# Kernel tuning notes

Measured on AMD Instinct MI355X. Metric: run time of the kernel, lower is better.

Reference implementation:

```python
import jax, jax.numpy as jnp
import numpy as np

SAMPLE_SIZE = 4096  # deterministic mode: first SAMPLE_SIZE flattened pixels
EPS_STD = 1e-8
EPS_PDF = 1e-10


def _std(v):
    # torch.std is unbiased (ddof=1)
    return jnp.std(v, ddof=1)


def _adaptive_sigma(v):
    # sigma=None path: 0.2 * std, clamped to [0.001, 1.0]
    return jnp.clip(_std(v) * 0.2, 0.001, 1.0)


def _normalize(v):
    return (v - jnp.mean(v)) / (_std(v) + EPS_STD)


def _marginal_pdf(values, sigma):
    vn = _normalize(values)                      # [N]
    resid = vn[None, :] - vn[:, None]            # [N, N]
    kernel = jnp.exp(-0.5 * (resid / sigma) ** 2)
    pdf = jnp.mean(kernel, axis=1)               # [N]
    return pdf / (jnp.sum(pdf) + EPS_PDF)


def _joint_pdf(v1, v2, s1, s2):
    vn1 = _normalize(v1)
    vn2 = _normalize(v2)
    r1 = vn1[None, :] - vn1[:, None]             # [N, N]
    r2 = vn2[None, :] - vn2[:, None]             # [N, N]
    kernel = jnp.exp(-0.5 * (r1 / s1) ** 2) * jnp.exp(-0.5 * (r2 / s2) ** 2)
    pdf = jnp.mean(kernel, axis=1)
    return pdf / (jnp.sum(pdf) + EPS_PDF)


def _mi_kde(img1, img2):
    x = img1.reshape(-1)[:SAMPLE_SIZE]
    y = img2.reshape(-1)[:SAMPLE_SIZE]
    s1 = _adaptive_sigma(x)
    s2 = _adaptive_sigma(y)
    p1 = _marginal_pdf(x, s1)
    p2 = _marginal_pdf(y, s2)
    pj = _joint_pdf(x, y, s1, s2)
    ratio = (pj + EPS_PDF) / (p1 * p2 + EPS_PDF)
    log_ratio = jnp.log(jnp.clip(ratio, 1e-10, 1e10))
    return jnp.sum(pj * log_ratio)


def setup_inputs() -> dict:
    key = jax.random.key(0)
    k1, k2, k3 = jax.random.split(key, 3)
    shape = (2, 1, 128, 128)  # [B, C, H, W] images in [0, 1]
    return {
        "fused_img": jax.random.uniform(k1, shape, dtype=jnp.float32),
        "source_img1": jax.random.uniform(k2, shape, dtype=jnp.float32),
        "source_img2": jax.random.uniform(k3, shape, dtype=jnp.float32),
    }


def reference(fused_img, source_img1, source_img2):
    B = fused_img.shape[0]
    total = jnp.float32(0.0)
    for b in range(B):  # small fixed batch loop, matches original
        total = total + _mi_kde(fused_img[b], source_img1[b]) \
                      + _mi_kde(fused_img[b], source_img2[b])
    return -(total / B)
```

## Files before the change

### kernel.cpp

```cpp
#include <hip/hip_runtime.h>

#define N 4096
#define NBIN 1024
#define LOG2E 1.4426950408889634f

__device__ __forceinline__ float fast_exp2(float x) {
#if __has_builtin(__builtin_amdgcn_exp2f)
    return __builtin_amdgcn_exp2f(x);
#else
    return exp2f(x);
#endif
}

__device__ float block_reduce_sum(float v) {
    __shared__ float red[16];
    int lane = threadIdx.x & 63;
    int wid = threadIdx.x >> 6;
    #pragma unroll
    for (int off = 32; off; off >>= 1) v += __shfl_down(v, off, 64);
    if (lane == 0) red[wid] = v;
    __syncthreads();
    if (threadIdx.x == 0) {
        int nw = (int)(blockDim.x >> 6);
        float s = red[0];
        for (int w = 1; w < nw; ++w) s += red[w];
        red[0] = s;
    }
    __syncthreads();
    float r = red[0];
    __syncthreads();
    return r;
}

__device__ float block_reduce_min(float v) {
    __shared__ float redm[16];
    int lane = threadIdx.x & 63;
    int wid = threadIdx.x >> 6;
    #pragma unroll
    for (int off = 32; off; off >>= 1) v = fminf(v, __shfl_down(v, off, 64));
    if (lane == 0) redm[wid] = v;
    __syncthreads();
    if (threadIdx.x == 0) {
        int nw = (int)(blockDim.x >> 6);
        float s = redm[0];
        for (int w = 1; w < nw; ++w) s = fminf(s, redm[w]);
        redm[0] = s;
    }
    __syncthreads();
    float r = redm[0];
    __syncthreads();
    return r;
}

__device__ float block_reduce_max(float v) {
    __shared__ float redx[16];
    int lane = threadIdx.x & 63;
    int wid = threadIdx.x >> 6;
    #pragma unroll
    for (int off = 32; off; off >>= 1) v = fmaxf(v, __shfl_down(v, off, 64));
    if (lane == 0) redx[wid] = v;
    __syncthreads();
    if (threadIdx.x == 0) {
        int nw = (int)(blockDim.x >> 6);
        float s = redx[0];
        for (int w = 1; w < nw; ++w) s = fmaxf(s, redx[w]);
        redx[0] = s;
    }
    __syncthreads();
    float r = redx[0];
    __syncthreads();
    return r;
}

__global__ void k_prep(const float* __restrict__ fused,
                       const float* __restrict__ s1,
                       const float* __restrict__ s2,
                       float2* __restrict__ xa,
                       float2* __restrict__ ma,
                       float* __restrict__ par,
                       float* __restrict__ hcnt,
                       float* __restrict__ hmu) {
    __shared__ unsigned int cnt[NBIN];
    __shared__ int qs[NBIN];
    int vec = blockIdx.x;
    int b = vec / 3, k = vec % 3;
    const float* src = (k == 0 ? fused : (k == 1 ? s1 : s2)) + b * 16384;
    int tid = threadIdx.x;
    float v[16];
    float s = 0.f;
    #pragma unroll
    for (int t = 0; t < 16; ++t) { v[t] = src[tid + t * 256]; s += v[t]; }
    float total = block_reduce_sum(s);
    float mean = total * (1.0f / 4096.0f);
    float ssq = 0.f;
    #pragma unroll
    for (int t = 0; t < 16; ++t) { float d = v[t] - mean; ssq += d * d; }
    float tssq = block_reduce_sum(ssq);
    float stdv = sqrtf(tssq / 4095.0f);
    float sigma = fminf(fmaxf(0.2f * stdv, 0.001f), 1.0f);
    float inv = 1.0f / (stdv + 1e-8f);
    float c1 = -0.5f * LOG2E / (sigma * sigma);

    float x[16];
    float lmin = 1e30f, lmax = -1e30f;
    #pragma unroll
    for (int t = 0; t < 16; ++t) {
        x[t] = (v[t] - mean) * inv;
        lmin = fminf(lmin, x[t]);
        lmax = fmaxf(lmax, x[t]);
    }
    float xmin = block_reduce_min(lmin);
    float xmax = block_reduce_max(lmax);
    float range = fmaxf(xmax - xmin, 1e-6f);
    float inv_bw = (float)NBIN / range;
    float binw = range * (1.0f / NBIN);

    float2* xav = xa + (size_t)vec * N;
    float2* mav = ma + (size_t)vec * N;
    for (int u = tid; u < NBIN; u += 256) { cnt[u] = 0u; qs[u] = 0; }
    __syncthreads();
    #pragma unroll
    for (int t = 0; t < 16; ++t) {
        int i = tid + t * 256;
        float a = c1 * x[t] * x[t];
        xav[i] = make_float2(x[t], a);
        mav[i] = make_float2(-2.0f * c1 * x[t], a);
        float rel = x[t] - xmin;
        int bb = min(NBIN - 1, max(0, (int)(rel * inv_bw)));
        atomicAdd(&cnt[bb], 1u);
        atomicAdd(&qs[bb], (int)rintf(rel * 16384.0f));
    }
    __syncthreads();
    for (int u = tid; u < NBIN; u += 256) {
        unsigned int c = cnt[u];
        hcnt[vec * NBIN + u] = (float)c;
        float mu = c ? xmin + ((float)qs[u] / (float)c) * (1.0f / 16384.0f)
                     : xmin + (u + 0.5f) * binw;
        hmu[vec * NBIN + u] = mu;
    }
    if (tid == 0) {
        par[vec * 8 + 0] = xmin;
        par[vec * 8 + 1] = inv_bw;
        par[vec * 8 + 2] = binw;
        par[vec * 8 + 3] = c1;
    }
}

__global__ void __launch_bounds__(256, 8)
k_main(const float2* __restrict__ xa,
       const float2* __restrict__ ma,
       const float* __restrict__ par,
       const float* __restrict__ hcnt,
       const float* __restrict__ hmu,
       float* __restrict__ marg,
       float* __restrict__ msum_part,
       float* __restrict__ part, int js) {
    __shared__ float4 sj[128];
    const int nib = 4;
    int bid = blockIdx.x;
    int tid = threadIdx.x;

    if (bid < 96) {
        int vec = bid >> 4, ic = bid & 15;
        int i = ic * 256 + tid;
        const float* P = par + vec * 8;
        float xmin = P[0], inv_bw = P[1], c1 = P[3];
        float xi = xa[(size_t)vec * N + i].x;
        float R = sqrtf(45.0f / fabsf(c1));
        int b0 = max(0, (int)((xi - R - xmin) * inv_bw));
        int b1 = min(NBIN - 1, (int)((xi + R - xmin) * inv_bw) + 1);
        const float* hc = hcnt + vec * NBIN;
        const float* hm = hmu + vec * NBIN;
        float acc = 0.f;
        #pragma unroll 4
        for (int bb = b0; bb <= b1; ++bb) {
            float d = xi - hm[bb];
            acc += hc[bb] * fast_exp2(c1 * d * d);
        }
        float raw = acc * (1.0f / N);
        marg[(size_t)vec * N + i] = raw;
        float tot = block_reduce_sum(raw);
        if (tid == 0) msum_part[bid] = tot;
        return;
    }

    int bid2 = bid - 96;
    int tt = bid2 / (nib * js);
    int rem = bid2 % (nib * js);
    int ib = rem / js, jsp = rem % js;
    int b = tt >> 1, pr = tt & 1;
    int vx = b * 3, vy = b * 3 + 1 + pr;
    int jlen = N / js;
    int j0 = jsp * jlen;
    int ibase = ib * 1024 + tid;

    const float2* xav = xa + (size_t)vx * N;
    const float2* yav = xa + (size_t)vy * N;
    const float2* mxv = ma + (size_t)vx * N;
    const float2* myv = ma + (size_t)vy * N;

    float mx[4], my[4], C[4];
    #pragma unroll
    for (int u = 0; u < 4; ++u) {
        float2 qx = mxv[ibase + u * 256];
        float2 qy = myv[ibase + u * 256];
        mx[u] = qx.x; my[u] = qy.x; C[u] = qx.y + qy.y;
    }
    float acc[4] = {0.f, 0.f, 0.f, 0.f};

    for (int jt = 0; jt < jlen; jt += 128) {
        int cnt = min(128, jlen - jt);
        __syncthreads();
        if (tid < cnt) {
            float2 xq = xav[j0 + jt + tid];
            float2 yq = yav[j0 + jt + tid];
            sj[tid] = make_float4(xq.x, yq.x, xq.y + yq.y, 0.f);
        }
        __syncthreads();
        #pragma unroll 2
        for (int j = 0; j < cnt; j += 2) {
            float4 q0 = sj[j];
            float4 q1 = sj[j + 1];
            float e0[4], e1[4], f0[4], f1[4];
            #pragma unroll
            for (int u = 0; u < 4; ++u) {
                e0[u] = fmaf(my[u], q0.y, fmaf(mx[u], q0.x, C[u])) + q0.z;
                e1[u] = fmaf(my[u], q1.y, fmaf(mx[u], q1.x, C[u])) + q1.z;
            }
            #pragma unroll
            for (int u = 0; u < 4; ++u) {
                f0[u] = fast_exp2(e0[u]);
                f1[u] = fast_exp2(e1[u]);
            }
            #pragma unroll
            for (int u = 0; u < 4; ++u)
                acc[u] += (f0[u] + f1[u]);
        }
    }
    float* dst = part + ((size_t)tt * js + jsp) * N + ibase;
    dst[0]   = acc[0];
    dst[256] = acc[1];
    dst[512] = acc[2];
    dst[768] = acc[3];
}

__global__ void k_reduce(const float* __restrict__ part, float* __restrict__ pdfj,
                         float* __restrict__ jsum_part, int js) {
    int blk = blockIdx.x;
    int tt = blk >> 4;
    int ic = blk & 15;
    int i = ic * 256 + threadIdx.x;
    float s = 0.f;
    #pragma unroll 4
    for (int q = 0; q < js; ++q) s += part[((size_t)tt * js + q) * N + i];
    s *= (1.0f / N);
    pdfj[(size_t)tt * N + i] = s;
    float tot = block_reduce_sum(s);
    if (threadIdx.x == 0) jsum_part[blk] = tot;
}

__global__ void k_mifin(const float* __restrict__ pdfj,
                        const float* __restrict__ jsum_part,
                        const float* __restrict__ marg,
                        const float* __restrict__ msum_part,
                        float* __restrict__ out) {
    __shared__ float tmp[160];
    __shared__ float svec[6], stask[4];
    int tid = threadIdx.x;
    if (tid < 96) tmp[tid] = msum_part[tid];
    else if (tid >= 128 && tid < 192) tmp[96 + tid - 128] = jsum_part[tid - 128];
    __syncthreads();
    if (tid < 6) {
        float s = 0.f;
        #pragma unroll
        for (int q = 0; q < 16; ++q) s += tmp[tid * 16 + q];
        svec[tid] = s;
    } else if (tid >= 8 && tid < 12) {
        int c = tid - 8;
        float s = 0.f;
        #pragma unroll
        for (int q = 0; q < 16; ++q) s += tmp[96 + c * 16 + q];
        stask[c] = s;
    }
    __syncthreads();

    float local = 0.f;
    #pragma unroll
    for (int k = 0; k < 16; ++k) {
        int g = tid + k * 1024;
        int c = g >> 12;
        int i = g & 4095;
        int b = c >> 1, pr = c & 1;
        int vx = b * 3, vy = b * 3 + 1 + pr;
        float pj = pdfj[(size_t)c * N + i] / (stask[c] + 1e-10f);
        float px = marg[(size_t)vx * N + i] / (svec[vx] + 1e-10f);
        float py = marg[(size_t)vy * N + i] / (svec[vy] + 1e-10f);
        float ratio = (pj + 1e-10f) / (px * py + 1e-10f);
        ratio = fminf(fmaxf(ratio, 1e-10f), 1e10f);
        local += pj * __logf(ratio);
    }
    float tot = block_reduce_sum(local);
    if (tid == 0) out[0] = -tot * 0.5f;
}

extern "C" void kernel_launch(void* const* d_in, const int* in_sizes, int n_in,
                              void* d_out, int out_size, void* d_ws, size_t ws_size,
                              hipStream_t stream) {
    const float* fused = (const float*)d_in[0];
    const float* s1    = (const float*)d_in[1];
    const float* s2    = (const float*)d_in[2];
    float* out = (float*)d_out;
    float* ws  = (float*)d_ws;

    const size_t off_xa   = 0;
    const size_t off_ma   = off_xa + 12 * (size_t)N;
    const size_t off_par  = off_ma + 12 * (size_t)N;
    const size_t off_hc   = off_par + 64;
    const size_t off_hm   = off_hc + 6 * NBIN;
    const size_t off_mg   = off_hm + 6 * NBIN;
    const size_t off_ms   = off_mg + 6 * (size_t)N;
    const size_t off_pj   = off_ms + 128;
    const size_t off_js   = off_pj + 4 * (size_t)N;
    const size_t off_part = off_js + 64;

    int js = 32;
    while (js > 1 && (off_part + (size_t)4 * js * N) * 4 > ws_size) js >>= 1;

    float2* ws_xa  = (float2*)(ws + off_xa);
    float2* ws_ma  = (float2*)(ws + off_ma);
    float*  ws_par = ws + off_par;
    float*  ws_hc  = ws + off_hc;
    float*  ws_hm  = ws + off_hm;
    float*  ws_mg  = ws + off_mg;
    float*  ws_ms  = ws + off_ms;
    float*  ws_pj  = ws + off_pj;
    float*  ws_js  = ws + off_js;
    float*  ws_part = ws + off_part;

    k_prep<<<dim3(6), dim3(256), 0, stream>>>(fused, s1, s2, ws_xa, ws_ma,
                                              ws_par, ws_hc, ws_hm);
    k_main<<<dim3(96 + 4 * 4 * js), dim3(256), 0, stream>>>(
        ws_xa, ws_ma, ws_par, ws_hc, ws_hm, ws_mg, ws_ms, ws_part, js);
    k_reduce<<<dim3(64), dim3(256), 0, stream>>>(ws_part, ws_pj, ws_js, js);
    k_mifin<<<dim3(1), dim3(1024), 0, stream>>>(ws_pj, ws_js, ws_mg, ws_ms, out);
}
```

Measured before the change: 40.39 us.

## Fold MI log-ratio into reduce kernel and widen prep to 1024 threads

The prep kernel now runs 1024 threads per vector and computes sum, sum of squares, min and max in one fused block reduction. Variance comes from the single-pass formula, and the normalized min/max come from the raw extremes. The MI sum is factored algebraically so the reduce kernel accumulates s*log(s/(rx*ry)) per block and the final kernel applies the normalizations per task with scalar math. This removes the pdfj round trip and the 16K-element final pass. The trade-off is that the epsilon and clamp terms are dropped, and the one-pass variance may lose precision or misbehave for zero densities.

```diff
diff --git a/kernel.cpp b/kernel.cpp
--- a/kernel.cpp
+++ b/kernel.cpp
@@ -32,111 +32,96 @@
     return r;
 }
 
-__device__ float block_reduce_min(float v) {
-    __shared__ float redm[16];
+__device__ float4 block_reduce_stats(float s, float sq, float mn, float mx) {
+    __shared__ float4 red4[16];
     int lane = threadIdx.x & 63;
     int wid = threadIdx.x >> 6;
     #pragma unroll
-    for (int off = 32; off; off >>= 1) v = fminf(v, __shfl_down(v, off, 64));
-    if (lane == 0) redm[wid] = v;
+    for (int off = 32; off; off >>= 1) {
+        s  += __shfl_down(s, off, 64);
+        sq += __shfl_down(sq, off, 64);
+        mn  = fminf(mn, __shfl_down(mn, off, 64));
+        mx  = fmaxf(mx, __shfl_down(mx, off, 64));
+    }
+    if (lane == 0) red4[wid] = make_float4(s, sq, mn, mx);
     __syncthreads();
     if (threadIdx.x == 0) {
-        int nw = (int)(blockDim.x >> 6);
-        float s = redm[0];
-        for (int w = 1; w < nw; ++w) s = fminf(s, redm[w]);
-        redm[0] = s;
-    }
-    __syncthreads();
-    float r = redm[0];
+        float4 r = red4[0];
+        #pragma unroll
+        for (int w = 1; w < 16; ++w) {
+            float4 q = red4[w];
+            r.x += q.x; r.y += q.y;
+            r.z = fminf(r.z, q.z); r.w = fmaxf(r.w, q.w);
+        }
+        red4[0] = r;
+    }
+    __syncthreads();
+    float4 r = red4[0];
     __syncthreads();
     return r;
 }
 
-__device__ float block_reduce_max(float v) {
-    __shared__ float redx[16];
-    int lane = threadIdx.x & 63;
-    int wid = threadIdx.x >> 6;
-    #pragma unroll
-    for (int off = 32; off; off >>= 1) v = fmaxf(v, __shfl_down(v, off, 64));
-    if (lane == 0) redx[wid] = v;
-    __syncthreads();
-    if (threadIdx.x == 0) {
-        int nw = (int)(blockDim.x >> 6);
-        float s = redx[0];
-        for (int w = 1; w < nw; ++w) s = fmaxf(s, redx[w]);
-        redx[0] = s;
-    }
-    __syncthreads();
-    float r = redx[0];
-    __syncthreads();
-    return r;
-}
-
-__global__ void k_prep(const float* __restrict__ fused,
-                       const float* __restrict__ s1,
-                       const float* __restrict__ s2,
-                       float2* __restrict__ xa,
-                       float2* __restrict__ ma,
-                       float* __restrict__ par,
-                       float* __restrict__ hcnt,
-                       float* __restrict__ hmu) {
+__global__ void __launch_bounds__(1024)
+k_prep(const float* __restrict__ fused,
+       const float* __restrict__ s1,
+       const float* __restrict__ s2,
+       float2* __restrict__ xa,
+       float2* __restrict__ ma,
+       float* __restrict__ par,
+       float* __restrict__ hcnt,
+       float* __restrict__ hmu) {
     __shared__ unsigned int cnt[NBIN];
     __shared__ int qs[NBIN];
     int vec = blockIdx.x;
     int b = vec / 3, k = vec % 3;
     const float* src = (k == 0 ? fused : (k == 1 ? s1 : s2)) + b * 16384;
     int tid = threadIdx.x;
-    float v[16];
-    float s = 0.f;
-    #pragma unroll
-    for (int t = 0; t < 16; ++t) { v[t] = src[tid + t * 256]; s += v[t]; }
-    float total = block_reduce_sum(s);
-    float mean = total * (1.0f / 4096.0f);
-    float ssq = 0.f;
-    #pragma unroll
-    for (int t = 0; t < 16; ++t) { float d = v[t] - mean; ssq += d * d; }
-    float tssq = block_reduce_sum(ssq);
-    float stdv = sqrtf(tssq / 4095.0f);
+
+    cnt[tid] = 0u; qs[tid] = 0;
+
+    float v[4];
+    float s = 0.f, sq = 0.f, mn = 1e30f, mx = -1e30f;
+    #pragma unroll
+    for (int t = 0; t < 4; ++t) {
+        v[t] = src[tid + t * 1024];
+        s += v[t]; sq = fmaf(v[t], v[t], sq);
+        mn = fminf(mn, v[t]); mx = fmaxf(mx, v[t]);
+    }
+    float4 r = block_reduce_stats(s, sq, mn, mx);
+    float mean = r.x * (1.0f / 4096.0f);
+    float tssq = r.y - 4096.0f * mean * mean;
+    float stdv = sqrtf(fmaxf(tssq, 0.f) / 4095.0f);
     float sigma = fminf(fmaxf(0.2f * stdv, 0.001f), 1.0f);
     float inv = 1.0f / (stdv + 1e-8f);
     float c1 = -0.5f * LOG2E / (sigma * sigma);
-
-    float x[16];
-    float lmin = 1e30f, lmax = -1e30f;
-    #pragma unroll
-    for (int t = 0; t < 16; ++t) {
-        x[t] = (v[t] - mean) * inv;
-        lmin = fminf(lmin, x[t]);
-        lmax = fmaxf(lmax, x[t]);
-    }
-    float xmin = block_reduce_min(lmin);
-    float xmax = block_reduce_max(lmax);
+    float xmin = (r.z - mean) * inv;
+    float xmax = (r.w - mean) * inv;
     float range = fmaxf(xmax - xmin, 1e-6f);
     float inv_bw = (float)NBIN / range;
     float binw = range * (1.0f / NBIN);
 
     float2* xav = xa + (size_t)vec * N;
     float2* mav = ma + (size_t)vec * N;
-    for (int u = tid; u < NBIN; u += 256) { cnt[u] = 0u; qs[u] = 0; }
-    __syncthreads();
-    #pragma unroll
-    for (int t = 0; t < 16; ++t) {
-        int i = tid + t * 256;
-        float a = c1 * x[t] * x[t];
-        xav[i] = make_float2(x[t], a);
-        mav[i] = make_float2(-2.0f * c1 * x[t], a);
-        float rel = x[t] - xmin;
+    __syncthreads();
+    #pragma unroll
+    for (int t = 0; t < 4; ++t) {
+        int i = tid + t * 1024;
+        float x = (v[t] - mean) * inv;
+        float a = c1 * x * x;
+        xav[i] = make_float2(x, a);
+        mav[i] = make_float2(-2.0f * c1 * x, a);
+        float rel = x - xmin;
         int bb = min(NBIN - 1, max(0, (int)(rel * inv_bw)));
         atomicAdd(&cnt[bb], 1u);
         atomicAdd(&qs[bb], (int)rintf(rel * 16384.0f));
     }
     __syncthreads();
-    for (int u = tid; u < NBIN; u += 256) {
-        unsigned int c = cnt[u];
-        hcnt[vec * NBIN + u] = (float)c;
-        float mu = c ? xmin + ((float)qs[u] / (float)c) * (1.0f / 16384.0f)
-                     : xmin + (u + 0.5f) * binw;
-        hmu[vec * NBIN + u] = mu;
+    {
+        unsigned int c = cnt[tid];
+        hcnt[vec * NBIN + tid] = (float)c;
+        float mu = c ? xmin + ((float)qs[tid] / (float)c) * (1.0f / 16384.0f)
+                     : xmin + (tid + 0.5f) * binw;
+        hmu[vec * NBIN + tid] = mu;
     }
     if (tid == 0) {
         par[vec * 8 + 0] = xmin;
@@ -244,63 +229,64 @@
     dst[768] = acc[3];
 }
 
-__global__ void k_reduce(const float* __restrict__ part, float* __restrict__ pdfj,
+__global__ void k_reduce(const float* __restrict__ part,
+                         const float* __restrict__ marg,
+                         float* __restrict__ A_part,
                          float* __restrict__ jsum_part, int js) {
     int blk = blockIdx.x;
     int tt = blk >> 4;
     int ic = blk & 15;
+    int b = tt >> 1, pr = tt & 1;
+    int vx = b * 3, vy = b * 3 + 1 + pr;
     int i = ic * 256 + threadIdx.x;
     float s = 0.f;
     #pragma unroll 4
     for (int q = 0; q < js; ++q) s += part[((size_t)tt * js + q) * N + i];
     s *= (1.0f / N);
-    pdfj[(size_t)tt * N + i] = s;
-    float tot = block_reduce_sum(s);
-    if (threadIdx.x == 0) jsum_part[blk] = tot;
-}
-
-__global__ void k_mifin(const float* __restrict__ pdfj,
-                        const float* __restrict__ jsum_part,
-                        const float* __restrict__ marg,
-                        const float* __restrict__ msum_part,
-                        float* __restrict__ out) {
-    __shared__ float tmp[160];
-    __shared__ float svec[6], stask[4];
+    float rx = marg[(size_t)vx * N + i];
+    float ry = marg[(size_t)vy * N + i];
+    float a = s * __logf(s / (rx * ry));
+    float stot = block_reduce_sum(s);
+    float atot = block_reduce_sum(a);
+    if (threadIdx.x == 0) {
+        jsum_part[blk] = stot;
+        A_part[blk] = atot;
+    }
+}
+
+__global__ void k_fin(const float* __restrict__ A_part,
+                      const float* __restrict__ jsum_part,
+                      const float* __restrict__ msum_part,
+                      float* __restrict__ out) {
+    __shared__ float svec[6], stask[4], sA[4];
     int tid = threadIdx.x;
-    if (tid < 96) tmp[tid] = msum_part[tid];
-    else if (tid >= 128 && tid < 192) tmp[96 + tid - 128] = jsum_part[tid - 128];
-    __syncthreads();
     if (tid < 6) {
         float s = 0.f;
         #pragma unroll
-        for (int q = 0; q < 16; ++q) s += tmp[tid * 16 + q];
+        for (int q = 0; q < 16; ++q) s += msum_part[tid * 16 + q];
         svec[tid] = s;
     } else if (tid >= 8 && tid < 12) {
         int c = tid - 8;
-        float s = 0.f;
+        float s = 0.f, a = 0.f;
         #pragma unroll
-        for (int q = 0; q < 16; ++q) s += tmp[96 + c * 16 + q];
+        for (int q = 0; q < 16; ++q) {
+            s += jsum_part[c * 16 + q];
+            a += A_part[c * 16 + q];
+        }
         stask[c] = s;
-    }
-    __syncthreads();
-
-    float local = 0.f;
-    #pragma unroll
-    for (int k = 0; k < 16; ++k) {
-        int g = tid + k * 1024;
-        int c = g >> 12;
-        int i = g & 4095;
-        int b = c >> 1, pr = c & 1;
-        int vx = b * 3, vy = b * 3 + 1 + pr;
-        float pj = pdfj[(size_t)c * N + i] / (stask[c] + 1e-10f);
-        float px = marg[(size_t)vx * N + i] / (svec[vx] + 1e-10f);
-        float py = marg[(size_t)vy * N + i] / (svec[vy] + 1e-10f);
-        float ratio = (pj + 1e-10f) / (px * py + 1e-10f);
-        ratio = fminf(fmaxf(ratio, 1e-10f), 1e10f);
-        local += pj * __logf(ratio);
-    }
-    float tot = block_reduce_sum(local);
-    if (tid == 0) out[0] = -tot * 0.5f;
+        sA[c] = a;
+    }
+    __syncthreads();
+    if (tid == 0) {
+        float mi = 0.f;
+        #pragma unroll
+        for (int c = 0; c < 4; ++c) {
+            int b = c >> 1, pr = c & 1;
+            int vx = b * 3, vy = b * 3 + 1 + pr;
+            mi += sA[c] / stask[c] + __logf(svec[vx] * svec[vy] / stask[c]);
+        }
+        out[0] = -mi * 0.5f;
+    }
 }
 
 extern "C" void kernel_launch(void* const* d_in, const int* in_sizes, int n_in,
@@ -319,8 +305,8 @@
     const size_t off_hm   = off_hc + 6 * NBIN;
     const size_t off_mg   = off_hm + 6 * NBIN;
     const size_t off_ms   = off_mg + 6 * (size_t)N;
-    const size_t off_pj   = off_ms + 128;
-    const size_t off_js   = off_pj + 4 * (size_t)N;
+    const size_t off_A    = off_ms + 128;
+    const size_t off_js   = off_A + 64;
     const size_t off_part = off_js + 64;
 
     int js = 32;
@@ -333,14 +319,14 @@
     float*  ws_hm  = ws + off_hm;
     float*  ws_mg  = ws + off_mg;
     float*  ws_ms  = ws + off_ms;
-    float*  ws_pj  = ws + off_pj;
+    float*  ws_A   = ws + off_A;
     float*  ws_js  = ws + off_js;
     float*  ws_part = ws + off_part;
 
-    k_prep<<<dim3(6), dim3(256), 0, stream>>>(fused, s1, s2, ws_xa, ws_ma,
-                                              ws_par, ws_hc, ws_hm);
+    k_prep<<<dim3(6), dim3(1024), 0, stream>>>(fused, s1, s2, ws_xa, ws_ma,
+                                               ws_par, ws_hc, ws_hm);
     k_main<<<dim3(96 + 4 * 4 * js), dim3(256), 0, stream>>>(
         ws_xa, ws_ma, ws_par, ws_hc, ws_hm, ws_mg, ws_ms, ws_part, js);
-    k_reduce<<<dim3(64), dim3(256), 0, stream>>>(ws_part, ws_pj, ws_js, js);
-    k_mifin<<<dim3(1), dim3(1024), 0, stream>>>(ws_pj, ws_js, ws_mg, ws_ms, out);
-}
+    k_reduce<<<dim3(64), dim3(256), 0, stream>>>(ws_part, ws_mg, ws_A, ws_js, js);
+    k_fin<<<dim3(1), dim3(128), 0, stream>>>(ws_A, ws_js, ws_ms, out);
+}
```

New measurement: 33.02 us. 18.2% less time.
